# Kernel optimization log

Hardware: AMD Instinct MI355X
Metric: run time of the kernel (lower is better)

The kernel has to match this reference:

```python
import jax, jax.numpy as jnp
import numpy as np

B, S, D_MODEL, D_K = 16, 2048, 64, 16
HEAD = D_MODEL * D_K  # 1024, width of each of q, k, v


def setup_inputs() -> dict:
    key = jax.random.key(0)
    kx, kw = jax.random.split(key)
    x = jax.random.normal(kx, (B, S, D_MODEL), dtype=jnp.float32)
    # flax Dense kernel: (in_features, features), no bias
    W = jax.random.normal(kw, (D_MODEL, 3 * HEAD), dtype=jnp.float32) / np.sqrt(D_MODEL)
    return {"x": x, "W": W}


def reference(x, W):
    # fused QKV projection (Dense, no bias)
    qkv = jnp.einsum("bsd,df->bsf", x, W)  # [B, S, 3*HEAD]
    q, k, v = jnp.split(qkv, 3, axis=-1)   # each [B, S, HEAD]

    # q @ k^T over the feature dim -> [B, S, S]
    attn = jnp.einsum("bqd,bkd->bqk", q, k)
    # NOTE: original code scales by sqrt(k.shape[0]) == batch size (kept faithfully)
    d_k = k.shape[0]
    attn = attn / jnp.sqrt(jnp.float32(d_k))
    # original masking: keep upper triangle, then send exact zeros to -9e15
    attn = jnp.triu(attn, k=0)
    attn = jnp.where(attn == 0, jnp.float32(-9000000000000000.0), attn)
    attn = jax.nn.softmax(attn, axis=-1)
    return jnp.einsum("bqk,bkd->bqd", attn, v)  # [B, S, HEAD]
```

## Files before the change

kernel.cpp:

```cpp
#include <hip/hip_runtime.h>
#include <math.h>

#define B_ 16
#define S_ 2048
#define DM_ 64
#define HD_ 1024

typedef float floatx4 __attribute__((ext_vector_type(4)));
typedef short bf16x8 __attribute__((ext_vector_type(8)));
typedef unsigned short ushort4v __attribute__((ext_vector_type(4)));
typedef unsigned short ushort8v __attribute__((ext_vector_type(8)));


__device__ __forceinline__ unsigned short bf_hi(float f) {
    return (unsigned short)((__float_as_uint(f) + 0x8000u) >> 16);
}
__device__ __forceinline__ float bf_f(unsigned short h) {
    return __uint_as_float((unsigned)h << 16);
}
__device__ __forceinline__ void cvt4(floatx4 v, ushort4v& h, ushort4v& l) {
    h[0] = bf_hi(v.x); l[0] = bf_hi(v.x - bf_f(h[0]));
    h[1] = bf_hi(v.y); l[1] = bf_hi(v.y - bf_f(h[1]));
    h[2] = bf_hi(v.z); l[2] = bf_hi(v.z - bf_f(h[2]));
    h[3] = bf_hi(v.w); l[3] = bf_hi(v.w - bf_f(h[3]));
}

#define MFMA(a, b, c) __builtin_amdgcn_mfma_f32_16x16x32_bf16((a), (b), (c), 0, 0, 0)

__global__ void k_M(const float* __restrict__ W, float* __restrict__ M) {
    const int d = blockIdx.x;
    const int e = threadIdx.x;
    const floatx4* wq = (const floatx4*)(W + (size_t)d * 3072);
    const floatx4* wk = (const floatx4*)(W + (size_t)e * 3072 + 1024);
    floatx4 a = {0.f, 0.f, 0.f, 0.f};
    for (int j = 0; j < 256; ++j) {
        floatx4 qv = wq[j], kv = wk[j];
        a.x = fmaf(qv.x, kv.x, a.x);
        a.y = fmaf(qv.y, kv.y, a.y);
        a.z = fmaf(qv.z, kv.z, a.z);
        a.w = fmaf(qv.w, kv.w, a.w);
    }
    M[d * 64 + e] = (a.x + a.y) + (a.z + a.w);
}

__global__ __launch_bounds__(256, 2) void k_y(
        const float* __restrict__ x, const float* __restrict__ M,
        float* __restrict__ y) {
    __shared__ __align__(16) float xs[128 * 64];
    const int tid = threadIdx.x;
    const int c   = tid & 63;
    const int g   = tid >> 6;
    const int r0  = blockIdx.x * 128;

    {
        const floatx4* src = (const floatx4*)(x + (size_t)r0 * 64);
        floatx4* dst = (floatx4*)xs;
#pragma unroll
        for (int i = 0; i < 8; ++i) dst[tid * 8 + i] = src[tid * 8 + i];
    }
    float mreg[64];
#pragma unroll
    for (int d = 0; d < 64; ++d) mreg[d] = M[d * 64 + c];
    __syncthreads();

    for (int r = 0; r < 32; ++r) {
        const int row = g * 32 + r;
        const floatx4* xr = (const floatx4*)(xs + row * 64);
        float a0 = 0.f, a1 = 0.f, a2 = 0.f, a3 = 0.f;
#pragma unroll
        for (int j = 0; j < 16; ++j) {
            floatx4 xv = xr[j];
            a0 = fmaf(xv.x, mreg[4 * j + 0], a0);
            a1 = fmaf(xv.y, mreg[4 * j + 1], a1);
            a2 = fmaf(xv.z, mreg[4 * j + 2], a2);
            a3 = fmaf(xv.w, mreg[4 * j + 3], a3);
        }
        y[(size_t)(r0 + row) * 64 + c] = (a0 + a1) + (a2 + a3);
    }
}

__global__ __launch_bounds__(512, 2) void k_attn4(
        const float* __restrict__ xg, const float* __restrict__ yg,
        float* __restrict__ Un) {
    __shared__ __align__(16) unsigned short sm[55296];

    const int tid  = threadIdx.x;
    const int h    = tid >> 8;
    const int lt   = tid & 255;
    const int w    = lt >> 6;
    const int lane = tid & 63;
    const int lm   = lane & 15;
    const int lg   = lane >> 4;

    const int bid = blockIdx.x;
    const int qt  = bid >> 4;
    const int bb  = bid & 15;
    const int q0  = qt * 64;
    const int T   = 32 - qt;
    const int nA  = (T + 1) >> 1;
    const int nOwn = h ? (T - nA) : nA;
    const int kt0  = q0 + (h ? nA * 64 : 0);

    unsigned short* base = sm + h * 23040;
    unsigned short* xrh = base;
    unsigned short* xrl = base + 4608;
    unsigned short* xth = base + 9216;
    unsigned short* xtl = base + 13824;
    unsigned short* Pw  = base + 18432 + w * 1152;
    unsigned short* yh  = sm + 46080;
    unsigned short* yl  = sm + 50688;

    {
        const int qrow = tid >> 3, part = tid & 7;
        const float* src = yg + ((size_t)bb * S_ + q0 + qrow) * 64 + part * 8;
        floatx4 a = *(const floatx4*)(src);
        floatx4 b = *(const floatx4*)(src + 4);
        ushort4v ha, la, hb, lb;
        cvt4(a, ha, la); cvt4(b, hb, lb);
        ushort8v hv = {ha[0], ha[1], ha[2], ha[3], hb[0], hb[1], hb[2], hb[3]};
        ushort8v lv = {la[0], la[1], la[2], la[3], lb[0], lb[1], lb[2], lb[3]};
        *(ushort8v*)(yh + qrow * 72 + part * 8) = hv;
        *(ushort8v*)(yl + qrow * 72 + part * 8) = lv;
    }

    const float* xb = xg + (size_t)bb * S_ * 64;
    const int kg = lt >> 4, dc = lt & 15;

    floatx4 v0, v1, v2, v3;
    if (0 < nOwn) {
        const float* sp = xb + (size_t)(kt0 + kg * 4) * 64 + dc * 4;
        v0 = *(const floatx4*)(sp);
        v1 = *(const floatx4*)(sp + 64);
        v2 = *(const floatx4*)(sp + 128);
        v3 = *(const floatx4*)(sp + 192);
    }

    __syncthreads();

    bf16x8 aqh[2], aql[2];
#pragma unroll
    for (int kc = 0; kc < 2; ++kc) {
        const int off = (16 * w + lm) * 72 + 32 * kc + 8 * lg;
        aqh[kc] = *(const bf16x8*)(yh + off);
        aql[kc] = *(const bf16x8*)(yl + off);
    }

    floatx4 U[4];
    float m[4], lsum[4];
#pragma unroll
    for (int r = 0; r < 4; ++r) { m[r] = -INFINITY; lsum[r] = 0.f; }
#pragma unroll
    for (int c = 0; c < 4; ++c) U[c] = (floatx4){0.f, 0.f, 0.f, 0.f};

    for (int t = 0; t < nA; ++t) {
        const int kt = kt0 + t * 64;
        __syncthreads();
        if (t < nOwn) {
            ushort4v h0, l0, h1, l1, h2, l2, h3, l3;
            cvt4(v0, h0, l0); cvt4(v1, h1, l1);
            cvt4(v2, h2, l2); cvt4(v3, h3, l3);
            *(ushort4v*)(xrh + (4 * kg + 0) * 72 + 4 * dc) = h0;
            *(ushort4v*)(xrh + (4 * kg + 1) * 72 + 4 * dc) = h1;
            *(ushort4v*)(xrh + (4 * kg + 2) * 72 + 4 * dc) = h2;
            *(ushort4v*)(xrh + (4 * kg + 3) * 72 + 4 * dc) = h3;
            *(ushort4v*)(xrl + (4 * kg + 0) * 72 + 4 * dc) = l0;
            *(ushort4v*)(xrl + (4 * kg + 1) * 72 + 4 * dc) = l1;
            *(ushort4v*)(xrl + (4 * kg + 2) * 72 + 4 * dc) = l2;
            *(ushort4v*)(xrl + (4 * kg + 3) * 72 + 4 * dc) = l3;
#pragma unroll
            for (int e = 0; e < 4; ++e) {
                ushort4v th = {h0[e], h1[e], h2[e], h3[e]};
                ushort4v tl = {l0[e], l1[e], l2[e], l3[e]};
                const int rT  = 4 * dc + e;
                const int off = rT * 72 + (((kg >> 1) ^ ((rT >> 3) & 3)) << 3)
                              + ((kg & 1) << 2);
                *(ushort4v*)(xth + off) = th;
                *(ushort4v*)(xtl + off) = tl;
            }
        }
        __syncthreads();

        if (t + 1 < nOwn) {
            const float* sp = xb + (size_t)(kt + 64 + kg * 4) * 64 + dc * 4;
            v0 = *(const floatx4*)(sp);
            v1 = *(const floatx4*)(sp + 64);
            v2 = *(const floatx4*)(sp + 128);
            v3 = *(const floatx4*)(sp + 192);
        }

        if (t < nOwn) {
            floatx4 Sc[4] = {{0.f,0.f,0.f,0.f},{0.f,0.f,0.f,0.f},
                             {0.f,0.f,0.f,0.f},{0.f,0.f,0.f,0.f}};
#pragma unroll
            for (int kc = 0; kc < 2; ++kc) {
#pragma unroll
                for (int c = 0; c < 4; ++c) {
                    const int ro = (lm + 16 * c) * 72 + 32 * kc + 8 * lg;
                    bf16x8 bh = *(const bf16x8*)(xrh + ro);
                    bf16x8 bl = *(const bf16x8*)(xrl + ro);
                    Sc[c] = MFMA(aqh[kc], bh, Sc[c]);
                    Sc[c] = MFMA(aqh[kc], bl, Sc[c]);
                    Sc[c] = MFMA(aql[kc], bh, Sc[c]);
                }
            }

            float p[4][4], alpha[4];
#pragma unroll
            for (int r = 0; r < 4; ++r) {
                const int ig = q0 + 16 * w + 4 * lg + r;
                float sv[4];
                float rmax = -INFINITY;
#pragma unroll
                for (int c = 0; c < 4; ++c) {
                    const int jg = kt + lm + 16 * c;
                    float v = Sc[c][r] * 0.25f;
                    if (jg < ig || v == 0.0f) v = -9.0e15f;
                    sv[c] = v;
                    rmax = fmaxf(rmax, v);
                }
                rmax = fmaxf(rmax, __shfl_xor(rmax, 1));
                rmax = fmaxf(rmax, __shfl_xor(rmax, 2));
                rmax = fmaxf(rmax, __shfl_xor(rmax, 4));
                rmax = fmaxf(rmax, __shfl_xor(rmax, 8));
                const float mnew = fmaxf(m[r], rmax);
                alpha[r] = __expf(m[r] - mnew);
                float ps = 0.f;
#pragma unroll
                for (int c = 0; c < 4; ++c) {
                    const float pv = __expf(sv[c] - mnew);
                    p[r][c] = pv;
                    ps += pv;
                }
                m[r] = mnew;
                lsum[r] = lsum[r] * alpha[r] + ps;
            }

#pragma unroll
            for (int r = 0; r < 4; ++r)
#pragma unroll
                for (int c = 0; c < 4; ++c)
                    Pw[(4 * lg + r) * 72 + lm + 16 * c] = bf_hi(p[r][c]);

            floatx4 av = {alpha[0], alpha[1], alpha[2], alpha[3]};
#pragma unroll
            for (int c = 0; c < 4; ++c) U[c] *= av;

#pragma unroll
            for (int kc = 0; kc < 2; ++kc) {
                bf16x8 ap = *(const bf16x8*)(Pw + lm * 72 + 32 * kc + 8 * lg);
#pragma unroll
                for (int c = 0; c < 4; ++c) {
                    const int d   = lm + 16 * c;
                    const int blk = (4 * kc + lg) ^ ((d >> 3) & 3);
                    const int off = d * 72 + blk * 8;
                    bf16x8 bh = *(const bf16x8*)(xth + off);
                    bf16x8 bl = *(const bf16x8*)(xtl + off);
                    U[c] = MFMA(ap, bh, U[c]);
                    U[c] = MFMA(ap, bl, U[c]);
                }
            }
        }
    }

    float lf[4];
#pragma unroll
    for (int r = 0; r < 4; ++r) {
        float s2 = lsum[r];
        s2 += __shfl_xor(s2, 1);
        s2 += __shfl_xor(s2, 2);
        s2 += __shfl_xor(s2, 4);
        s2 += __shfl_xor(s2, 8);
        lf[r] = s2;
    }

    __syncthreads();
    float* sc = (float*)sm;
    if (h == 1) {
        float* bp = sc + lt * 24;
        *(floatx4*)(bp)     = (floatx4){m[0], m[1], m[2], m[3]};
        *(floatx4*)(bp + 4) = (floatx4){lf[0], lf[1], lf[2], lf[3]};
#pragma unroll
        for (int c = 0; c < 4; ++c) *(floatx4*)(bp + 8 + 4 * c) = U[c];
    }
    __syncthreads();
    if (h == 0) {
        const float* bp = sc + lt * 24;
        floatx4 mB = *(const floatx4*)(bp);
        floatx4 lB = *(const floatx4*)(bp + 4);
        floatx4 UB[4];
#pragma unroll
        for (int c = 0; c < 4; ++c) UB[c] = *(const floatx4*)(bp + 8 + 4 * c);
        float eA[4], eB[4], inv[4];
#pragma unroll
        for (int r = 0; r < 4; ++r) {
            const float mT = fmaxf(m[r], mB[r]);
            eA[r] = __expf(m[r] - mT);
            eB[r] = __expf(mB[r] - mT);
            const float lT = lf[r] * eA[r] + lB[r] * eB[r];
            inv[r] = 1.0f / lT;
        }
#pragma unroll
        for (int r = 0; r < 4; ++r) {
            const size_t row = (size_t)bb * S_ + q0 + 16 * w + 4 * lg + r;
#pragma unroll
            for (int c = 0; c < 4; ++c)
                Un[row * 64 + lm + 16 * c] =
                    (U[c][r] * eA[r] + UB[c][r] * eB[r]) * inv[r];
        }
    }
}

__global__ __launch_bounds__(256, 2) void k_out(
        const float* __restrict__ Un, const float* __restrict__ W,
        float* __restrict__ out) {
    __shared__ __align__(16) float us[64 * 64];
    const int tid = threadIdx.x;
    const int r0  = (blockIdx.x >> 1) * 64;
    const int cb  = (blockIdx.x & 1) * 512;
    const int c0  = cb + tid;

    float w0[64], w1[64];
#pragma unroll
    for (int d = 0; d < 64; ++d) {
        w0[d] = W[(size_t)d * 3072 + 2048 + c0];
        w1[d] = W[(size_t)d * 3072 + 2048 + c0 + 256];
    }
    {
        const floatx4* src = (const floatx4*)(Un + (size_t)r0 * 64);
        floatx4* dst = (floatx4*)us;
#pragma unroll
        for (int i = 0; i < 4; ++i) dst[tid * 4 + i] = src[tid * 4 + i];
    }
    __syncthreads();

    for (int row = 0; row < 64; ++row) {
        const floatx4* ur = (const floatx4*)(us + row * 64);
        float a0 = 0.f, a1 = 0.f;
#pragma unroll
        for (int j = 0; j < 16; ++j) {
            floatx4 u = ur[j];
            a0 = fmaf(u.x, w0[4 * j + 0], a0); a1 = fmaf(u.x, w1[4 * j + 0], a1);
            a0 = fmaf(u.y, w0[4 * j + 1], a0); a1 = fmaf(u.y, w1[4 * j + 1], a1);
            a0 = fmaf(u.z, w0[4 * j + 2], a0); a1 = fmaf(u.z, w1[4 * j + 2], a1);
            a0 = fmaf(u.w, w0[4 * j + 3], a0); a1 = fmaf(u.w, w1[4 * j + 3], a1);
        }
        float* op = out + (size_t)(r0 + row) * HD_ + c0;
        op[0]   = a0;
        op[256] = a1;
    }
}

extern "C" void kernel_launch(void* const* d_in, const int* in_sizes, int n_in,
                              void* d_out, int out_size, void* d_ws, size_t ws_size,
                              hipStream_t stream) {
    const float* x = (const float*)d_in[0];
    const float* W = (const float*)d_in[1];
    float* out = (float*)d_out;

    float* M  = (float*)d_ws;
    float* y  = M + 4096;
    float* Un = y + (size_t)32768 * 64;

    k_M    <<<dim3(64),   64,  0, stream>>>(W, M);
    k_y    <<<dim3(256),  256, 0, stream>>>(x, M, y);
    k_attn4<<<dim3(512),  512, 0, stream>>>(x, y, Un);
    k_out  <<<dim3(1024), 256, 0, stream>>>(Un, W, out);
}
```

Measured before the change: 264.6 us.

## Fuse query projection and output projection into attention kernel using split-bf16 MFMA

Collapses four kernels into two. A small prep kernel computes M = Wq·Wkᵀ and reorders both M and the Wv slice into bf16 hi/lo MFMA fragment layout. The attention kernel now computes y = x·M per tile with MFMA from the first staged x tile, and applies the Wv output projection in registers via MFMA before writing the final output. This removes the y and Un round trips through global memory and two launches. It also restructures the per-tile staging so the next tile is written at the end of each iteration, and changes launch bounds to 1 block per CU. The cost is extra MFMA and register pressure in the fused kernel and a 3-term bf16 split approximation for the projections.

```diff
diff --git a/kernel.cpp b/kernel.cpp
--- a/kernel.cpp
+++ b/kernel.cpp
@@ -27,67 +27,86 @@
 
 #define MFMA(a, b, c) __builtin_amdgcn_mfma_f32_16x16x32_bf16((a), (b), (c), 0, 0, 0)
 
-__global__ void k_M(const float* __restrict__ W, float* __restrict__ M) {
-    const int d = blockIdx.x;
-    const int e = threadIdx.x;
-    const floatx4* wq = (const floatx4*)(W + (size_t)d * 3072);
-    const floatx4* wk = (const floatx4*)(W + (size_t)e * 3072 + 1024);
-    floatx4 a = {0.f, 0.f, 0.f, 0.f};
-    for (int j = 0; j < 256; ++j) {
-        floatx4 qv = wq[j], kv = wk[j];
-        a.x = fmaf(qv.x, kv.x, a.x);
-        a.y = fmaf(qv.y, kv.y, a.y);
-        a.z = fmaf(qv.z, kv.z, a.z);
-        a.w = fmaf(qv.w, kv.w, a.w);
-    }
-    M[d * 64 + e] = (a.x + a.y) + (a.z + a.w);
-}
-
-__global__ __launch_bounds__(256, 2) void k_y(
-        const float* __restrict__ x, const float* __restrict__ M,
-        float* __restrict__ y) {
-    __shared__ __align__(16) float xs[128 * 64];
-    const int tid = threadIdx.x;
-    const int c   = tid & 63;
-    const int g   = tid >> 6;
-    const int r0  = blockIdx.x * 128;
-
-    {
-        const floatx4* src = (const floatx4*)(x + (size_t)r0 * 64);
-        floatx4* dst = (floatx4*)xs;
-#pragma unroll
-        for (int i = 0; i < 8; ++i) dst[tid * 8 + i] = src[tid * 8 + i];
-    }
-    float mreg[64];
-#pragma unroll
-    for (int d = 0; d < 64; ++d) mreg[d] = M[d * 64 + c];
-    __syncthreads();
-
-    for (int r = 0; r < 32; ++r) {
-        const int row = g * 32 + r;
-        const floatx4* xr = (const floatx4*)(xs + row * 64);
-        float a0 = 0.f, a1 = 0.f, a2 = 0.f, a3 = 0.f;
-#pragma unroll
-        for (int j = 0; j < 16; ++j) {
-            floatx4 xv = xr[j];
-            a0 = fmaf(xv.x, mreg[4 * j + 0], a0);
-            a1 = fmaf(xv.y, mreg[4 * j + 1], a1);
-            a2 = fmaf(xv.z, mreg[4 * j + 2], a2);
-            a3 = fmaf(xv.w, mreg[4 * j + 3], a3);
-        }
-        y[(size_t)(r0 + row) * 64 + c] = (a0 + a1) + (a2 + a3);
-    }
-}
-
-__global__ __launch_bounds__(512, 2) void k_attn4(
-        const float* __restrict__ xg, const float* __restrict__ yg,
-        float* __restrict__ Un) {
+__device__ __forceinline__ int fragidx(int k, int col) {
+    return (((col >> 4) * 2 + (k >> 5)) * 64 + ((k >> 3) & 3) * 16 + (col & 15)) * 8
+           + (k & 7);
+}
+
+__global__ void k_prep(const float* __restrict__ W, unsigned short* __restrict__ ws) {
+    unsigned short* Mfh = ws;
+    unsigned short* Mfl = ws + 4096;
+    unsigned short* Wfh = ws + 8192;
+    unsigned short* Wfl = ws + 73728;
+    const int bid = blockIdx.x, t = threadIdx.x;
+    if (bid < 64) {
+        const int d = bid;
+        const int e = t;
+        const floatx4* wq = (const floatx4*)(W + (size_t)d * 3072);
+        const floatx4* wk = (const floatx4*)(W + (size_t)e * 3072 + 1024);
+        floatx4 a = {0.f, 0.f, 0.f, 0.f};
+#pragma unroll 4
+        for (int j = 0; j < 256; ++j) {
+            floatx4 qv = wq[j], kv = wk[j];
+            a.x = fmaf(qv.x, kv.x, a.x);
+            a.y = fmaf(qv.y, kv.y, a.y);
+            a.z = fmaf(qv.z, kv.z, a.z);
+            a.w = fmaf(qv.w, kv.w, a.w);
+        }
+        const float v = (a.x + a.y) + (a.z + a.w);
+        const int idx = fragidx(d, e);
+        const unsigned short hv = bf_hi(v);
+        Mfh[idx] = hv;
+        Mfl[idx] = bf_hi(v - bf_f(hv));
+    } else {
+        const int col = (bid - 64) * 64 + t;
+#pragma unroll 8
+        for (int k = 0; k < 64; ++k) {
+            const float v = W[(size_t)k * 3072 + 2048 + col];
+            const int idx = fragidx(k, col);
+            const unsigned short hv = bf_hi(v);
+            Wfh[idx] = hv;
+            Wfl[idx] = bf_hi(v - bf_f(hv));
+        }
+    }
+}
+
+__device__ __forceinline__ void stage_tile(
+        unsigned short* xrh, unsigned short* xrl,
+        unsigned short* xth, unsigned short* xtl,
+        int kg, int dc, floatx4 v0, floatx4 v1, floatx4 v2, floatx4 v3) {
+    ushort4v h0, l0, h1, l1, h2, l2, h3, l3;
+    cvt4(v0, h0, l0); cvt4(v1, h1, l1);
+    cvt4(v2, h2, l2); cvt4(v3, h3, l3);
+    *(ushort4v*)(xrh + (4 * kg + 0) * 72 + 4 * dc) = h0;
+    *(ushort4v*)(xrh + (4 * kg + 1) * 72 + 4 * dc) = h1;
+    *(ushort4v*)(xrh + (4 * kg + 2) * 72 + 4 * dc) = h2;
+    *(ushort4v*)(xrh + (4 * kg + 3) * 72 + 4 * dc) = h3;
+    *(ushort4v*)(xrl + (4 * kg + 0) * 72 + 4 * dc) = l0;
+    *(ushort4v*)(xrl + (4 * kg + 1) * 72 + 4 * dc) = l1;
+    *(ushort4v*)(xrl + (4 * kg + 2) * 72 + 4 * dc) = l2;
+    *(ushort4v*)(xrl + (4 * kg + 3) * 72 + 4 * dc) = l3;
+#pragma unroll
+    for (int e = 0; e < 4; ++e) {
+        ushort4v th = {h0[e], h1[e], h2[e], h3[e]};
+        ushort4v tl = {l0[e], l1[e], l2[e], l3[e]};
+        const int rT  = 4 * dc + e;
+        const int off = rT * 72 + (((kg >> 1) ^ ((rT >> 3) & 3)) << 3)
+                      + ((kg & 1) << 2);
+        *(ushort4v*)(xth + off) = th;
+        *(ushort4v*)(xtl + off) = tl;
+    }
+}
+
+__global__ __launch_bounds__(512, 1) void k_fused(
+        const float* __restrict__ xg, const unsigned short* __restrict__ wsf,
+        float* __restrict__ out) {
     __shared__ __align__(16) unsigned short sm[55296];
 
     const int tid  = threadIdx.x;
     const int h    = tid >> 8;
     const int lt   = tid & 255;
     const int w    = lt >> 6;
+    const int wid  = tid >> 6;
     const int lane = tid & 63;
     const int lm   = lane & 15;
     const int lg   = lane >> 4;
@@ -110,18 +129,10 @@
     unsigned short* yh  = sm + 46080;
     unsigned short* yl  = sm + 50688;
 
-    {
-        const int qrow = tid >> 3, part = tid & 7;
-        const float* src = yg + ((size_t)bb * S_ + q0 + qrow) * 64 + part * 8;
-        floatx4 a = *(const floatx4*)(src);
-        floatx4 b = *(const floatx4*)(src + 4);
-        ushort4v ha, la, hb, lb;
-        cvt4(a, ha, la); cvt4(b, hb, lb);
-        ushort8v hv = {ha[0], ha[1], ha[2], ha[3], hb[0], hb[1], hb[2], hb[3]};
-        ushort8v lv = {la[0], la[1], la[2], la[3], lb[0], lb[1], lb[2], lb[3]};
-        *(ushort8v*)(yh + qrow * 72 + part * 8) = hv;
-        *(ushort8v*)(yl + qrow * 72 + part * 8) = lv;
-    }
+    const unsigned short* Mfh = wsf;
+    const unsigned short* Mfl = wsf + 4096;
+    const unsigned short* Wfh = wsf + 8192;
+    const unsigned short* Wfl = wsf + 73728;
 
     const float* xb = xg + (size_t)bb * S_ * 64;
     const int kg = lt >> 4, dc = lt & 15;
@@ -133,8 +144,49 @@
         v1 = *(const floatx4*)(sp + 64);
         v2 = *(const floatx4*)(sp + 128);
         v3 = *(const floatx4*)(sp + 192);
-    }
-
+        stage_tile(xrh, xrl, xth, xtl, kg, dc, v0, v1, v2, v3);
+    }
+    if (1 < nOwn) {
+        const float* sp = xb + (size_t)(kt0 + 64 + kg * 4) * 64 + dc * 4;
+        v0 = *(const floatx4*)(sp);
+        v1 = *(const floatx4*)(sp + 64);
+        v2 = *(const floatx4*)(sp + 128);
+        v3 = *(const floatx4*)(sp + 192);
+    }
+    __syncthreads();
+
+    {
+        const int rt = wid & 3;
+        const int cp = wid >> 2;
+        bf16x8 axh[2], axl[2];
+#pragma unroll
+        for (int kc = 0; kc < 2; ++kc) {
+            const int off = (16 * rt + lm) * 72 + 32 * kc + 8 * lg;
+            axh[kc] = *(const bf16x8*)(sm + off);
+            axl[kc] = *(const bf16x8*)(sm + 4608 + off);
+        }
+#pragma unroll
+        for (int cc = 0; cc < 2; ++cc) {
+            const int ct = cp * 2 + cc;
+            floatx4 yC = {0.f, 0.f, 0.f, 0.f};
+#pragma unroll
+            for (int kc = 0; kc < 2; ++kc) {
+                bf16x8 bh = *(const bf16x8*)(Mfh + ((ct * 2 + kc) * 64 + lane) * 8);
+                bf16x8 bl = *(const bf16x8*)(Mfl + ((ct * 2 + kc) * 64 + lane) * 8);
+                yC = MFMA(axh[kc], bh, yC);
+                yC = MFMA(axh[kc], bl, yC);
+                yC = MFMA(axl[kc], bh, yC);
+            }
+#pragma unroll
+            for (int r = 0; r < 4; ++r) {
+                const float vv = yC[r];
+                const unsigned short hv = bf_hi(vv);
+                const int o = (16 * rt + 4 * lg + r) * 72 + ct * 16 + lm;
+                yh[o] = hv;
+                yl[o] = bf_hi(vv - bf_f(hv));
+            }
+        }
+    }
     __syncthreads();
 
     bf16x8 aqh[2], aql[2];
@@ -154,40 +206,6 @@
 
     for (int t = 0; t < nA; ++t) {
         const int kt = kt0 + t * 64;
-        __syncthreads();
-        if (t < nOwn) {
-            ushort4v h0, l0, h1, l1, h2, l2, h3, l3;
-            cvt4(v0, h0, l0); cvt4(v1, h1, l1);
-            cvt4(v2, h2, l2); cvt4(v3, h3, l3);
-            *(ushort4v*)(xrh + (4 * kg + 0) * 72 + 4 * dc) = h0;
-            *(ushort4v*)(xrh + (4 * kg + 1) * 72 + 4 * dc) = h1;
-            *(ushort4v*)(xrh + (4 * kg + 2) * 72 + 4 * dc) = h2;
-            *(ushort4v*)(xrh + (4 * kg + 3) * 72 + 4 * dc) = h3;
-            *(ushort4v*)(xrl + (4 * kg + 0) * 72 + 4 * dc) = l0;
-            *(ushort4v*)(xrl + (4 * kg + 1) * 72 + 4 * dc) = l1;
-            *(ushort4v*)(xrl + (4 * kg + 2) * 72 + 4 * dc) = l2;
-            *(ushort4v*)(xrl + (4 * kg + 3) * 72 + 4 * dc) = l3;
-#pragma unroll
-            for (int e = 0; e < 4; ++e) {
-                ushort4v th = {h0[e], h1[e], h2[e], h3[e]};
-                ushort4v tl = {l0[e], l1[e], l2[e], l3[e]};
-                const int rT  = 4 * dc + e;
-                const int off = rT * 72 + (((kg >> 1) ^ ((rT >> 3) & 3)) << 3)
-                              + ((kg & 1) << 2);
-                *(ushort4v*)(xth + off) = th;
-                *(ushort4v*)(xtl + off) = tl;
-            }
-        }
-        __syncthreads();
-
-        if (t + 1 < nOwn) {
-            const float* sp = xb + (size_t)(kt + 64 + kg * 4) * 64 + dc * 4;
-            v0 = *(const floatx4*)(sp);
-            v1 = *(const floatx4*)(sp + 64);
-            v2 = *(const floatx4*)(sp + 128);
-            v3 = *(const floatx4*)(sp + 192);
-        }
-
         if (t < nOwn) {
             floatx4 Sc[4] = {{0.f,0.f,0.f,0.f},{0.f,0.f,0.f,0.f},
                              {0.f,0.f,0.f,0.f},{0.f,0.f,0.f,0.f}};
@@ -260,6 +278,20 @@
                 }
             }
         }
+
+        if (t + 1 < nA) {
+            __syncthreads();
+            if (t + 1 < nOwn)
+                stage_tile(xrh, xrl, xth, xtl, kg, dc, v0, v1, v2, v3);
+            if (t + 2 < nOwn) {
+                const float* sp = xb + (size_t)(kt + 128 + kg * 4) * 64 + dc * 4;
+                v0 = *(const floatx4*)(sp);
+                v1 = *(const floatx4*)(sp + 64);
+                v2 = *(const floatx4*)(sp + 128);
+                v3 = *(const floatx4*)(sp + 192);
+            }
+            __syncthreads();
+        }
     }
 
     float lf[4];
@@ -275,6 +307,8 @@
 
     __syncthreads();
     float* sc = (float*)sm;
+    unsigned short* Unh = sm + 23040;
+    unsigned short* Unl = sm + 27648;
     if (h == 1) {
         float* bp = sc + lt * 24;
         *(floatx4*)(bp)     = (floatx4){m[0], m[1], m[2], m[3]};
@@ -300,53 +334,48 @@
             inv[r] = 1.0f / lT;
         }
 #pragma unroll
-        for (int r = 0; r < 4; ++r) {
-            const size_t row = (size_t)bb * S_ + q0 + 16 * w + 4 * lg + r;
-#pragma unroll
-            for (int c = 0; c < 4; ++c)
-                Un[row * 64 + lm + 16 * c] =
-                    (U[c][r] * eA[r] + UB[c][r] * eB[r]) * inv[r];
-        }
-    }
-}
-
-__global__ __launch_bounds__(256, 2) void k_out(
-        const float* __restrict__ Un, const float* __restrict__ W,
-        float* __restrict__ out) {
-    __shared__ __align__(16) float us[64 * 64];
-    const int tid = threadIdx.x;
-    const int r0  = (blockIdx.x >> 1) * 64;
-    const int cb  = (blockIdx.x & 1) * 512;
-    const int c0  = cb + tid;
-
-    float w0[64], w1[64];
-#pragma unroll
-    for (int d = 0; d < 64; ++d) {
-        w0[d] = W[(size_t)d * 3072 + 2048 + c0];
-        w1[d] = W[(size_t)d * 3072 + 2048 + c0 + 256];
-    }
-    {
-        const floatx4* src = (const floatx4*)(Un + (size_t)r0 * 64);
-        floatx4* dst = (floatx4*)us;
-#pragma unroll
-        for (int i = 0; i < 4; ++i) dst[tid * 4 + i] = src[tid * 4 + i];
-    }
-    __syncthreads();
-
-    for (int row = 0; row < 64; ++row) {
-        const floatx4* ur = (const floatx4*)(us + row * 64);
-        float a0 = 0.f, a1 = 0.f;
-#pragma unroll
-        for (int j = 0; j < 16; ++j) {
-            floatx4 u = ur[j];
-            a0 = fmaf(u.x, w0[4 * j + 0], a0); a1 = fmaf(u.x, w1[4 * j + 0], a1);
-            a0 = fmaf(u.y, w0[4 * j + 1], a0); a1 = fmaf(u.y, w1[4 * j + 1], a1);
-            a0 = fmaf(u.z, w0[4 * j + 2], a0); a1 = fmaf(u.z, w1[4 * j + 2], a1);
-            a0 = fmaf(u.w, w0[4 * j + 3], a0); a1 = fmaf(u.w, w1[4 * j + 3], a1);
-        }
-        float* op = out + (size_t)(r0 + row) * HD_ + c0;
-        op[0]   = a0;
-        op[256] = a1;
+        for (int r = 0; r < 4; ++r)
+#pragma unroll
+            for (int c = 0; c < 4; ++c) {
+                const float o = (U[c][r] * eA[r] + UB[c][r] * eB[r]) * inv[r];
+                const unsigned short hv = bf_hi(o);
+                const int oo = (16 * w + 4 * lg + r) * 72 + lm + 16 * c;
+                Unh[oo] = hv;
+                Unl[oo] = bf_hi(o - bf_f(hv));
+            }
+    }
+    __syncthreads();
+
+    bf16x8 Ah[4][2], Al[4][2];
+#pragma unroll
+    for (int rt = 0; rt < 4; ++rt)
+#pragma unroll
+        for (int kc = 0; kc < 2; ++kc) {
+            const int off = (16 * rt + lm) * 72 + 32 * kc + 8 * lg;
+            Ah[rt][kc] = *(const bf16x8*)(Unh + off);
+            Al[rt][kc] = *(const bf16x8*)(Unl + off);
+        }
+    const size_t orow0 = (size_t)bb * S_ + q0;
+#pragma unroll
+    for (int ctl = 0; ctl < 8; ++ctl) {
+        const int ct = wid * 8 + ctl;
+        bf16x8 Bh0 = *(const bf16x8*)(Wfh + ((ct * 2 + 0) * 64 + lane) * 8);
+        bf16x8 Bl0 = *(const bf16x8*)(Wfl + ((ct * 2 + 0) * 64 + lane) * 8);
+        bf16x8 Bh1 = *(const bf16x8*)(Wfh + ((ct * 2 + 1) * 64 + lane) * 8);
+        bf16x8 Bl1 = *(const bf16x8*)(Wfl + ((ct * 2 + 1) * 64 + lane) * 8);
+#pragma unroll
+        for (int rt = 0; rt < 4; ++rt) {
+            floatx4 C = {0.f, 0.f, 0.f, 0.f};
+            C = MFMA(Ah[rt][0], Bh0, C);
+            C = MFMA(Ah[rt][0], Bl0, C);
+            C = MFMA(Al[rt][0], Bh0, C);
+            C = MFMA(Ah[rt][1], Bh1, C);
+            C = MFMA(Ah[rt][1], Bl1, C);
+            C = MFMA(Al[rt][1], Bh1, C);
+#pragma unroll
+            for (int r = 0; r < 4; ++r)
+                out[(orow0 + 16 * rt + 4 * lg + r) * HD_ + ct * 16 + lm] = C[r];
+        }
     }
 }
 
@@ -355,14 +384,8 @@
                               hipStream_t stream) {
     const float* x = (const float*)d_in[0];
     const float* W = (const float*)d_in[1];
-    float* out = (float*)d_out;
-
-    float* M  = (float*)d_ws;
-    float* y  = M + 4096;
-    float* Un = y + (size_t)32768 * 64;
-
-    k_M    <<<dim3(64),   64,  0, stream>>>(W, M);
-    k_y    <<<dim3(256),  256, 0, stream>>>(x, M, y);
-    k_attn4<<<dim3(512),  512, 0, stream>>>(x, y, Un);
-    k_out  <<<dim3(1024), 256, 0, stream>>>(Un, W, out);
-}
+    unsigned short* wsf = (unsigned short*)d_ws;
+
+    k_prep <<<dim3(80),  64,  0, stream>>>(W, wsf);
+    k_fused<<<dim3(512), 512, 0, stream>>>(x, wsf, (float*)d_out);
+}
```

Result: faster. 232.4 us (-12.2%).
